# Kernel tuning notes

Measured on AMD Instinct MI355X. Metric: run time of the kernel, lower is better.

## Reference

```python
import jax, jax.numpy as jnp
import numpy as np

D_MODEL = 1024
N_HEADS = 16
HEAD_DIM = D_MODEL // N_HEADS
D_FF = 4096
MAX_STEPS = 16
MAX_LEN = 64  # hardcoded in the module
LN_EPS = 1e-5


def _layer_norm(x, g, b):
    m = jnp.mean(x, axis=-1, keepdims=True)
    v = jnp.mean((x - m) ** 2, axis=-1, keepdims=True)
    return (x - m) * jax.lax.rsqrt(v + LN_EPS) * g + b


def setup_inputs() -> dict:
    key = jax.random.key(0)
    ks = jax.random.split(key, 12)
    B, S = 8, 1024
    std = 0.02
    return {
        "x": jax.random.normal(ks[0], (B, S, D_MODEL), dtype=jnp.float32),
        "step_embed": jax.random.normal(ks[1], (MAX_STEPS, D_MODEL), dtype=jnp.float32) * std,
        "qkv_w": jax.random.normal(ks[2], (D_MODEL, 3 * D_MODEL), dtype=jnp.float32) * std,
        "qkv_b": jnp.zeros((3 * D_MODEL,), dtype=jnp.float32),
        "out_w": jax.random.normal(ks[3], (D_MODEL, D_MODEL), dtype=jnp.float32) * std,
        "out_b": jnp.zeros((D_MODEL,), dtype=jnp.float32),
        "rel_pos_bias": jax.random.normal(ks[4], (2 * MAX_LEN - 1,), dtype=jnp.float32) * std,
        "w1": jax.random.normal(ks[5], (D_MODEL, D_FF), dtype=jnp.float32) * std,
        "b1": jnp.zeros((D_FF,), dtype=jnp.float32),
        "w2": jax.random.normal(ks[6], (D_FF, D_MODEL), dtype=jnp.float32) * std,
        "b2": jnp.zeros((D_MODEL,), dtype=jnp.float32),
        "ln1_g": jnp.ones((D_MODEL,), dtype=jnp.float32),
        "ln1_b": jnp.zeros((D_MODEL,), dtype=jnp.float32),
        "ln2_g": jnp.ones((D_MODEL,), dtype=jnp.float32),
        "ln2_b": jnp.zeros((D_MODEL,), dtype=jnp.float32),
        "think_step": 3,
    }


def reference(x, step_embed, qkv_w, qkv_b, out_w, out_b, rel_pos_bias,
              w1, b1, w2, b2, ln1_g, ln1_b, ln2_g, ln2_b, think_step):
    B, S, D = x.shape
    scale = HEAD_DIM ** -0.5

    # step embedding (clamped), broadcast over batch and sequence
    step = min(int(think_step), MAX_STEPS - 1)
    x = x + step_embed[step][None, None, :]

    # QKV projection -> (3, B, H, S, Dh)
    qkv = (x @ qkv_w + qkv_b).reshape(B, S, 3, N_HEADS, HEAD_DIM)
    qkv = jnp.transpose(qkv, (2, 0, 3, 1, 4))
    q, k, v = qkv[0], qkv[1], qkv[2]

    # attention scores with clamped relative-position bias
    scores = jnp.einsum("bhqd,bhkd->bhqk", q, k) * scale
    pos = jnp.arange(S)
    rel = jnp.clip(pos[:, None] - pos[None, :] + (MAX_LEN - 1), 0, 2 * MAX_LEN - 2)
    scores = scores + rel_pos_bias[rel][None, None, :, :]

    probs = jax.nn.softmax(scores, axis=-1)
    attn = jnp.einsum("bhqk,bhkd->bhqd", probs, v)
    attn = jnp.transpose(attn, (0, 2, 1, 3)).reshape(B, S, D)
    attn = attn @ out_w + out_b

    x = _layer_norm(x + attn, ln1_g, ln1_b)
    ffn = jax.nn.gelu(x @ w1 + b1, approximate=False) @ w2 + b2
    x = _layer_norm(x + ffn, ln2_g, ln2_b)
    return x
```

## Files before the change

### kernel.cpp

```cpp
#include <hip/hip_runtime.h>
#include <cstdint>
#include <cmath>

typedef unsigned short u16;
typedef unsigned int u32;
typedef __bf16 bf16x8 __attribute__((ext_vector_type(8)));
typedef float f32x4 __attribute__((ext_vector_type(4)));
typedef float f32x16 __attribute__((ext_vector_type(16)));

#define DEV __device__ __forceinline__

DEV u16 f2bf(float f) {
    union { float f; unsigned u; } a; a.f = f;
    unsigned u = a.u;
    return (u16)((u + 0x7FFFu + ((u >> 16) & 1u)) >> 16);
}

DEV u32 pack2bf(float a, float b) {
    union { float f; u32 u; } ua, ub; ua.f = a; ub.f = b;
    return __builtin_amdgcn_perm(ub.u + 0x8000u, ua.u + 0x8000u, 0x07060302u);
}

DEV float fast_exp2(float x) {
    float r;
    asm("v_exp_f32 %0, %1" : "=v"(r) : "v"(x));
    return r;
}

DEV void async16(void* lds, const void* g) {
    __builtin_amdgcn_global_load_lds(
        (const __attribute__((address_space(1))) unsigned int*)g,
        (__attribute__((address_space(3))) unsigned int*)lds, 16, 0, 0);
}

#define LOG2E 1.44269504088896f

__global__ void transpose_all(const float* __restrict__ s0, u16* __restrict__ d0,
                              const float* __restrict__ s1, u16* __restrict__ d1,
                              const float* __restrict__ s2, u16* __restrict__ d2,
                              const float* __restrict__ s3, u16* __restrict__ d3) {
    __shared__ float tile[32][33];
    int b = blockIdx.x;
    const float* src; u16* dst; int N, tidx;
    if (b < 3072)      { src = s0; dst = d0; N = 3072; tidx = b; }
    else if (b < 4096) { src = s1; dst = d1; N = 1024; tidx = b - 3072; }
    else if (b < 8192) { src = s2; dst = d2; N = 4096; tidx = b - 4096; }
    else               { src = s3; dst = d3; N = 1024; tidx = b - 8192; }
    int ntx = N >> 5;
    int n0 = (tidx % ntx) * 32, k0 = (tidx / ntx) * 32;
    int K = (b >= 8192) ? 4096 : 1024;
    int tx = threadIdx.x, ty = threadIdx.y;
    #pragma unroll
    for (int i = ty; i < 32; i += 8) tile[i][tx] = src[(size_t)(k0 + i) * N + n0 + tx];
    __syncthreads();
    #pragma unroll
    for (int i = ty; i < 32; i += 8) dst[(size_t)(n0 + i) * K + k0 + tx] = f2bf(tile[tx][i]);
}

__global__ __launch_bounds__(256)
void add_step_k(const float* __restrict__ x, const float* __restrict__ se,
                const int* __restrict__ ts, float* __restrict__ xo, u16* __restrict__ xb) {
    int st = ts[0]; st = st < 0 ? 0 : (st > 15 ? 15 : st);
    size_t i = (size_t)blockIdx.x * 256 + threadIdx.x;
    float4 v = ((const float4*)x)[i];
    int c = (int)(i & 255);
    float4 e = ((const float4*)(se + (size_t)st * 1024))[c];
    v.x += e.x; v.y += e.y; v.z += e.z; v.w += e.w;
    ((float4*)xo)[i] = v;
    ushort4 u; u.x = f2bf(v.x); u.y = f2bf(v.y); u.z = f2bf(v.z); u.w = f2bf(v.w);
    ((ushort4*)xb)[i] = u;
}

template<int EPI>
__global__ __launch_bounds__(256)
void gemm_bt(const u16* __restrict__ A, const u16* __restrict__ Bt,
             const float* __restrict__ bias, int Kdim,
             u16* __restrict__ ob0, u16* __restrict__ ob1, u16* __restrict__ ob2,
             const float* __restrict__ addf, float* __restrict__ outf) {
    __shared__ __align__(16) u16 lA[128 * 64];
    __shared__ __align__(16) u16 lB[128 * 64];
    const int tid = threadIdx.x, wave = tid >> 6, lane = tid & 63;
    const int m5 = lane & 31, h = lane >> 5;
    const int wm = wave >> 1, wn = wave & 1;
    const size_t m0 = (size_t)blockIdx.x * 128, n0 = (size_t)blockIdx.y * 128;
    const size_t kb = (size_t)Kdim * 2;

    f32x16 acc[2][2];
    #pragma unroll
    for (int i = 0; i < 2; i++)
        #pragma unroll
        for (int j = 0; j < 2; j++)
            #pragma unroll
            for (int e = 0; e < 16; e++) acc[i][j][e] = 0.f;

    const char* Ab = (const char*)A + m0 * kb;
    const char* Bb = (const char*)Bt + n0 * kb;

    auto stage = [&](const char* srcbase, u16* ldsb, int k0) {
        #pragma unroll
        for (int j = 0; j < 4; j++) {
            int loff = wave * 4096 + j * 1024 + lane * 16;
            int L = loff >> 4, r = L >> 3, c = L & 7, g = c ^ (r & 7);
            async16((char*)ldsb + loff, srcbase + (size_t)r * kb + (size_t)k0 * 2 + g * 16);
        }
    };

    stage(Ab, lA, 0); stage(Bb, lB, 0);
    const int r7 = m5 & 7;
    for (int k0 = 0; k0 < Kdim; k0 += 64) {
        __syncthreads();
        bf16x8 af[2][4], bfr[2][4];
        #pragma unroll
        for (int ti = 0; ti < 2; ti++) {
            int rowA = wm * 64 + ti * 32 + m5;
            int rowB = wn * 64 + ti * 32 + m5;
            #pragma unroll
            for (int kh = 0; kh < 4; kh++) {
                int cs = (kh * 2 + h) ^ r7;
                af[ti][kh]  = *(const bf16x8*)((const char*)lA + rowA * 128 + cs * 16);
                bfr[ti][kh] = *(const bf16x8*)((const char*)lB + rowB * 128 + cs * 16);
            }
        }
        __syncthreads();
        if (k0 + 64 < Kdim) { stage(Ab, lA, k0 + 64); stage(Bb, lB, k0 + 64); }
        #pragma unroll
        for (int kh = 0; kh < 4; kh++)
            #pragma unroll
            for (int ti = 0; ti < 2; ti++)
                #pragma unroll
                for (int tj = 0; tj < 2; tj++)
                    acc[ti][tj] = __builtin_amdgcn_mfma_f32_32x32x16_bf16(
                        af[ti][kh], bfr[tj][kh], acc[ti][tj], 0, 0, 0);
    }

    #pragma unroll
    for (int ti = 0; ti < 2; ti++) {
        #pragma unroll
        for (int tj = 0; tj < 2; tj++) {
            size_t col = n0 + wn * 64 + tj * 32 + m5;
            float bv = bias[col];
            if constexpr (EPI == 0) {
                size_t t = col >> 10, c = col & 1023, hh = c >> 6, dh = c & 63;
                #pragma unroll
                for (int g = 0; g < 4; g++) {
                    size_t row0 = m0 + wm * 64 + ti * 32 + 4 * h + 8 * g;
                    size_t bq = row0 >> 10, s0 = row0 & 1023;
                    if (t == 0) {
                        #pragma unroll
                        for (int r = 0; r < 4; r++)
                            ob0[((bq * 16 + hh) * 1024 + s0 + r) * 64 + dh] =
                                f2bf((acc[ti][tj][g * 4 + r] + bv) * 0.18033688011112f);
                    } else if (t == 1) {
                        #pragma unroll
                        for (int r = 0; r < 4; r++)
                            ob1[((bq * 16 + hh) * 1024 + s0 + r) * 64 + dh] =
                                f2bf(acc[ti][tj][g * 4 + r] + bv);
                    } else {
                        ushort4 tmp;
                        tmp.x = f2bf(acc[ti][tj][g * 4 + 0] + bv);
                        tmp.y = f2bf(acc[ti][tj][g * 4 + 1] + bv);
                        tmp.z = f2bf(acc[ti][tj][g * 4 + 2] + bv);
                        tmp.w = f2bf(acc[ti][tj][g * 4 + 3] + bv);
                        *(ushort4*)(ob2 + ((bq * 16 + hh) * 64 + dh) * 1024 + s0) = tmp;
                    }
                }
            } else {
                #pragma unroll
                for (int g = 0; g < 4; g++) {
                    #pragma unroll
                    for (int r = 0; r < 4; r++) {
                        size_t row = m0 + wm * 64 + ti * 32 + 4 * h + 8 * g + r;
                        float val = acc[ti][tj][g * 4 + r] + bv;
                        if constexpr (EPI == 1) {
                            size_t o = row * 1024 + col;
                            outf[o] = addf[o] + val;
                        } else if constexpr (EPI == 2) {
                            float ge = 0.5f * val * (1.f + erff(val * 0.70710678118f));
                            ob0[row * 4096 + col] = f2bf(ge);
                        } else {
                            size_t o = row * 1024 + col;
                            outf[o] = addf[o] + val;
                        }
                    }
                }
            }
        }
    }
}

__global__ __launch_bounds__(256)
void attn_k(const u16* __restrict__ Q, const u16* __restrict__ K_, const u16* __restrict__ Vt,
            const float* __restrict__ relb, u16* __restrict__ Out) {
    __shared__ __align__(16) u16 sP[64 * 128];
    __shared__ __align__(16) u16 sK[128 * 64];
    __shared__ __align__(16) u16 sVt[64 * 128];
    __shared__ float sRel[128];

    const int tid = threadIdx.x, wave = tid >> 6, lane = tid & 63;
    const int quad = lane >> 4, l15 = lane & 15;
    const int sw8 = l15 & 7;
    const int bh = blockIdx.x, q0 = blockIdx.y * 64;
    const size_t base = (size_t)bh * 65536;

    if (tid < 127) sRel[tid] = relb[tid] * LOG2E;

    auto stageK = [&](int kv0) {
        const char* kbp = (const char*)(K_ + base + (size_t)kv0 * 64);
        #pragma unroll
        for (int j = 0; j < 4; j++) {
            int loff = wave * 4096 + j * 1024 + lane * 16;
            int L = loff >> 4, r = L >> 3, c = L & 7, g = c ^ (r & 7);
            async16((char*)sK + loff, kbp + (size_t)r * 128 + g * 16);
        }
    };
    auto stageV = [&](int kv0) {
        const char* vbp = (const char*)(Vt + base) + (size_t)kv0 * 2;
        #pragma unroll
        for (int j = 0; j < 4; j++) {
            int loff = wave * 4096 + j * 1024 + lane * 16;
            int L = loff >> 4, r = L >> 4, c = L & 15, g = c ^ (r & 15);
            async16((char*)sVt + loff, vbp + (size_t)r * 2048 + g * 16);
        }
    };

    {
        const char* qb = (const char*)(Q + base + (size_t)q0 * 64);
        #pragma unroll
        for (int j = 0; j < 2; j++) {
            int loff = wave * 2048 + j * 1024 + lane * 16;
            int L = loff >> 4, r = L >> 3, c = L & 7, g = c ^ (r & 7);
            async16((char*)sP + loff, qb + (size_t)r * 128 + g * 16);
        }
    }
    stageK(0); stageV(0);
    __syncthreads();

    const int rowQ = wave * 16 + l15;
    bf16x8 aq0 = *(const bf16x8*)((const char*)sP + rowQ * 128 + ((quad ^ sw8) * 16));
    bf16x8 aq1 = *(const bf16x8*)((const char*)sP + rowQ * 128 + (((4 + quad) ^ sw8) * 16));

    bf16x8 ones;
    {
        union { short s[8]; bf16x8 v; } ou;
        #pragma unroll
        for (int i = 0; i < 8; i++) ou.s[i] = 0x3F80;
        ones = ou.v;
    }

    f32x4 Oacc[4], lsum;
    #pragma unroll
    for (int n = 0; n < 4; n++) Oacc[n] = f32x4{0.f, 0.f, 0.f, 0.f};
    lsum = f32x4{0.f, 0.f, 0.f, 0.f};

    for (int t = 0; t < 8; t++) {
        const int kv0 = t * 128;
        f32x4 sc[8];
        #pragma unroll
        for (int ni = 0; ni < 8; ni++) {
            const char* kr = (const char*)sK + (ni * 16 + l15) * 128;
            bf16x8 k0f = *(const bf16x8*)(kr + ((quad ^ sw8) * 16));
            bf16x8 k1f = *(const bf16x8*)(kr + (((4 + quad) ^ sw8) * 16));
            f32x4 z = f32x4{0.f, 0.f, 0.f, 0.f};
            z = __builtin_amdgcn_mfma_f32_16x16x32_bf16(k0f, aq0, z, 0, 0, 0);
            sc[ni] = __builtin_amdgcn_mfma_f32_16x16x32_bf16(k1f, aq1, z, 0, 0, 0);
        }
        const int qs = q0 + rowQ;
        if (kv0 >= q0 + 126) {
            float cb = sRel[0];
            #pragma unroll
            for (int ni = 0; ni < 8; ni++)
                #pragma unroll
                for (int r = 0; r < 4; r++) sc[ni][r] = fast_exp2(sc[ni][r] + cb);
        } else if (kv0 <= q0 - 190) {
            float cb = sRel[126];
            #pragma unroll
            for (int ni = 0; ni < 8; ni++)
                #pragma unroll
                for (int r = 0; r < 4; r++) sc[ni][r] = fast_exp2(sc[ni][r] + cb);
        } else {
            #pragma unroll
            for (int ni = 0; ni < 8; ni++) {
                #pragma unroll
                for (int r = 0; r < 4; r++) {
                    int ks = kv0 + ni * 16 + quad * 4 + r;
                    int rel = qs - ks + 63;
                    rel = rel < 0 ? 0 : (rel > 126 ? 126 : rel);
                    sc[ni][r] = fast_exp2(sc[ni][r] + sRel[rel]);
                }
            }
        }
        {
            char* prow = (char*)sP + rowQ * 256 + (quad & 1) * 8;
            #pragma unroll
            for (int ni = 0; ni < 8; ni++) {
                uint2 pk;
                pk.x = pack2bf(sc[ni][0], sc[ni][1]);
                pk.y = pack2bf(sc[ni][2], sc[ni][3]);
                int c16 = (ni * 2 + (quad >> 1)) ^ l15;
                *(uint2*)(prow + c16 * 16) = pk;
            }
        }
        __syncthreads();
        if (t < 7) stageK(kv0 + 128);

        #pragma unroll
        for (int kk = 0; kk < 4; kk++) {
            int swc = (kk * 4 + quad) ^ l15;
            bf16x8 pf = *(const bf16x8*)((const char*)sP + rowQ * 256 + swc * 16);
            lsum = __builtin_amdgcn_mfma_f32_16x16x32_bf16(pf, ones, lsum, 0, 0, 0);
            #pragma unroll
            for (int n = 0; n < 4; n++) {
                bf16x8 vf = *(const bf16x8*)((const char*)sVt + (n * 16 + l15) * 256 + swc * 16);
                Oacc[n] = __builtin_amdgcn_mfma_f32_16x16x32_bf16(pf, vf, Oacc[n], 0, 0, 0);
            }
        }
        __syncthreads();
        if (t < 7) stageV(kv0 + 128);
    }

    const int b = bh >> 4, hh = bh & 15;
    #pragma unroll
    for (int r = 0; r < 4; r++) {
        float inv = 1.f / lsum[r];
        int srow = q0 + wave * 16 + quad * 4 + r;
        size_t rowg = ((size_t)b * 1024 + srow) * 1024 + hh * 64;
        #pragma unroll
        for (int n = 0; n < 4; n++) Out[rowg + n * 16 + l15] = f2bf(Oacc[n][r] * inv);
    }
}

template<bool WB>
__global__ __launch_bounds__(256)
void ln_k(const float* __restrict__ in, const float* __restrict__ g, const float* __restrict__ b,
          float* __restrict__ of, u16* __restrict__ ob) {
    __shared__ float ws1[4], ws2[4];
    int row = blockIdx.x, t = threadIdx.x;
    float4 v = ((const float4*)(in + (size_t)row * 1024))[t];
    float s = v.x + v.y + v.z + v.w;
    float s2 = v.x * v.x + v.y * v.y + v.z * v.z + v.w * v.w;
    #pragma unroll
    for (int m = 1; m < 64; m <<= 1) { s += __shfl_xor(s, m); s2 += __shfl_xor(s2, m); }
    if ((t & 63) == 0) { ws1[t >> 6] = s; ws2[t >> 6] = s2; }
    __syncthreads();
    s = ws1[0] + ws1[1] + ws1[2] + ws1[3];
    s2 = ws2[0] + ws2[1] + ws2[2] + ws2[3];
    float mean = s * (1.f / 1024.f);
    float var = s2 * (1.f / 1024.f) - mean * mean;
    float inv = rsqrtf(var + 1e-5f);
    float4 gv = ((const float4*)g)[t], bv = ((const float4*)b)[t];
    float4 o;
    o.x = (v.x - mean) * inv * gv.x + bv.x;
    o.y = (v.y - mean) * inv * gv.y + bv.y;
    o.z = (v.z - mean) * inv * gv.z + bv.z;
    o.w = (v.w - mean) * inv * gv.w + bv.w;
    ((float4*)(of + (size_t)row * 1024))[t] = o;
    if (WB) {
        ushort4 u; u.x = f2bf(o.x); u.y = f2bf(o.y); u.z = f2bf(o.z); u.w = f2bf(o.w);
        ((ushort4*)(ob + (size_t)row * 1024))[t] = u;
    }
}

extern "C" void kernel_launch(void* const* d_in, const int* in_sizes, int n_in,
                              void* d_out, int out_size, void* d_ws, size_t ws_size,
                              hipStream_t stream) {
    (void)in_sizes; (void)n_in; (void)out_size; (void)ws_size;
    const float* x          = (const float*)d_in[0];
    const float* step_embed = (const float*)d_in[1];
    const float* qkv_w      = (const float*)d_in[2];
    const float* qkv_b      = (const float*)d_in[3];
    const float* out_w      = (const float*)d_in[4];
    const float* out_b      = (const float*)d_in[5];
    const float* relb       = (const float*)d_in[6];
    const float* w1         = (const float*)d_in[7];
    const float* b1         = (const float*)d_in[8];
    const float* w2         = (const float*)d_in[9];
    const float* b2         = (const float*)d_in[10];
    const float* ln1g       = (const float*)d_in[11];
    const float* ln1b       = (const float*)d_in[12];
    const float* ln2g       = (const float*)d_in[13];
    const float* ln2b       = (const float*)d_in[14];
    const int*   tstep      = (const int*)d_in[15];
    float* out = (float*)d_out;

    char* p = (char*)d_ws;
    u16* wt_qkv = (u16*)p; p += (size_t)3072 * 1024 * 2;
    u16* wt_out = (u16*)p; p += (size_t)1024 * 1024 * 2;
    u16* wt_w1  = (u16*)p; p += (size_t)4096 * 1024 * 2;
    u16* wt_w2  = (u16*)p; p += (size_t)1024 * 4096 * 2;
    float* xse  = (float*)p; p += (size_t)8192 * 1024 * 4;
    u16* xseb   = (u16*)p; p += (size_t)8192 * 1024 * 2;
    u16* qbuf   = (u16*)p; p += (size_t)8192 * 1024 * 2;
    u16* kbuf   = (u16*)p; p += (size_t)8192 * 1024 * 2;
    u16* attnb  = (u16*)p; p += (size_t)8192 * 1024 * 2;
    float* res1 = (float*)p; p += (size_t)8192 * 1024 * 4;
    float* y1   = xse;
    u16*   y1b  = xseb;
    u16*   hbuf = qbuf;
    float* res2 = res1;
    u16*   vtb  = (u16*)res1;

    transpose_all<<<dim3(12288), dim3(32, 8), 0, stream>>>(qkv_w, wt_qkv, out_w, wt_out,
                                                           w1, wt_w1, w2, wt_w2);
    add_step_k<<<dim3(8192), dim3(256), 0, stream>>>(x, step_embed, tstep, xse, xseb);
    gemm_bt<0><<<dim3(64, 24), dim3(256), 0, stream>>>(xseb, wt_qkv, qkv_b, 1024,
                                                       qbuf, kbuf, vtb, (const float*)nullptr, (float*)nullptr);
    attn_k<<<dim3(128, 16), dim3(256), 0, stream>>>(qbuf, kbuf, vtb, relb, attnb);
    gemm_bt<1><<<dim3(64, 8), dim3(256), 0, stream>>>(attnb, wt_out, out_b, 1024,
                                                      (u16*)nullptr, (u16*)nullptr, (u16*)nullptr, xse, res1);
    ln_k<true><<<dim3(8192), dim3(256), 0, stream>>>(res1, ln1g, ln1b, y1, y1b);
    gemm_bt<2><<<dim3(64, 32), dim3(256), 0, stream>>>(y1b, wt_w1, b1, 1024,
                                                       hbuf, (u16*)nullptr, (u16*)nullptr, (const float*)nullptr, (float*)nullptr);
    gemm_bt<3><<<dim3(64, 8), dim3(256), 0, stream>>>(hbuf, wt_w2, b2, 4096,
                                                      (u16*)nullptr, (u16*)nullptr, (u16*)nullptr, y1, res2);
    ln_k<false><<<dim3(8192), dim3(256), 0, stream>>>(res2, ln2g, ln2b, out, (u16*)nullptr);
}
```

Measured before the change: 530.2 us.

## Restructure attention to 128-query tiles with 32x32 MFMA and merge prep kernels

The attention kernel now processes 128 queries per block instead of 64, halving the grid and the number of times K/V tiles are loaded per head. It switches to 32x32x16 MFMA instructions, splits the work so each wave computes scores for a 32-key slice and later accumulates P·V for a 64-query by 32-dim output slice, and computes row sums directly with a cross-wave LDS reduction. The weight transpose and step-embedding add are fused into one launch to save a kernel launch. Risks are higher register pressure from holding 16 Q fragments and larger LDS use, which could lower occupancy.

```diff
diff --git a/kernel.cpp b/kernel.cpp
--- a/kernel.cpp
+++ b/kernel.cpp
@@ -35,40 +35,41 @@
 
 #define LOG2E 1.44269504088896f
 
-__global__ void transpose_all(const float* __restrict__ s0, u16* __restrict__ d0,
-                              const float* __restrict__ s1, u16* __restrict__ d1,
-                              const float* __restrict__ s2, u16* __restrict__ d2,
-                              const float* __restrict__ s3, u16* __restrict__ d3) {
-    __shared__ float tile[32][33];
-    int b = blockIdx.x;
-    const float* src; u16* dst; int N, tidx;
-    if (b < 3072)      { src = s0; dst = d0; N = 3072; tidx = b; }
-    else if (b < 4096) { src = s1; dst = d1; N = 1024; tidx = b - 3072; }
-    else if (b < 8192) { src = s2; dst = d2; N = 4096; tidx = b - 4096; }
-    else               { src = s3; dst = d3; N = 1024; tidx = b - 8192; }
-    int ntx = N >> 5;
-    int n0 = (tidx % ntx) * 32, k0 = (tidx / ntx) * 32;
-    int K = (b >= 8192) ? 4096 : 1024;
-    int tx = threadIdx.x, ty = threadIdx.y;
-    #pragma unroll
-    for (int i = ty; i < 32; i += 8) tile[i][tx] = src[(size_t)(k0 + i) * N + n0 + tx];
-    __syncthreads();
-    #pragma unroll
-    for (int i = ty; i < 32; i += 8) dst[(size_t)(n0 + i) * K + k0 + tx] = f2bf(tile[tx][i]);
-}
-
 __global__ __launch_bounds__(256)
-void add_step_k(const float* __restrict__ x, const float* __restrict__ se,
-                const int* __restrict__ ts, float* __restrict__ xo, u16* __restrict__ xb) {
-    int st = ts[0]; st = st < 0 ? 0 : (st > 15 ? 15 : st);
-    size_t i = (size_t)blockIdx.x * 256 + threadIdx.x;
-    float4 v = ((const float4*)x)[i];
-    int c = (int)(i & 255);
-    float4 e = ((const float4*)(se + (size_t)st * 1024))[c];
-    v.x += e.x; v.y += e.y; v.z += e.z; v.w += e.w;
-    ((float4*)xo)[i] = v;
-    ushort4 u; u.x = f2bf(v.x); u.y = f2bf(v.y); u.z = f2bf(v.z); u.w = f2bf(v.w);
-    ((ushort4*)xb)[i] = u;
+void prep_k(const float* __restrict__ s0, u16* __restrict__ d0,
+            const float* __restrict__ s1, u16* __restrict__ d1,
+            const float* __restrict__ s2, u16* __restrict__ d2,
+            const float* __restrict__ s3, u16* __restrict__ d3,
+            const float* __restrict__ x, const float* __restrict__ se,
+            const int* __restrict__ ts, float* __restrict__ xo, u16* __restrict__ xb) {
+    int b = blockIdx.x, tid = threadIdx.x;
+    if (b < 12288) {
+        __shared__ float tile[32][33];
+        const float* src; u16* dst; int N, tidx;
+        if (b < 3072)      { src = s0; dst = d0; N = 3072; tidx = b; }
+        else if (b < 4096) { src = s1; dst = d1; N = 1024; tidx = b - 3072; }
+        else if (b < 8192) { src = s2; dst = d2; N = 4096; tidx = b - 4096; }
+        else               { src = s3; dst = d3; N = 1024; tidx = b - 8192; }
+        int ntx = N >> 5;
+        int n0 = (tidx % ntx) * 32, k0 = (tidx / ntx) * 32;
+        int K = (b >= 8192) ? 4096 : 1024;
+        int tx = tid & 31, ty = tid >> 5;
+        #pragma unroll
+        for (int i = ty; i < 32; i += 8) tile[i][tx] = src[(size_t)(k0 + i) * N + n0 + tx];
+        __syncthreads();
+        #pragma unroll
+        for (int i = ty; i < 32; i += 8) dst[(size_t)(n0 + i) * K + k0 + tx] = f2bf(tile[tx][i]);
+    } else {
+        int st = ts[0]; st = st < 0 ? 0 : (st > 15 ? 15 : st);
+        size_t i = (size_t)(b - 12288) * 256 + tid;
+        float4 v = ((const float4*)x)[i];
+        int c = (int)(i & 255);
+        float4 e = ((const float4*)(se + (size_t)st * 1024))[c];
+        v.x += e.x; v.y += e.y; v.z += e.z; v.w += e.w;
+        ((float4*)xo)[i] = v;
+        ushort4 u; u.x = f2bf(v.x); u.y = f2bf(v.y); u.z = f2bf(v.z); u.w = f2bf(v.w);
+        ((ushort4*)xb)[i] = u;
+    }
 }
 
 template<int EPI>
@@ -188,18 +189,19 @@
     }
 }
 
-__global__ __launch_bounds__(256)
+__global__ __launch_bounds__(256, 2)
 void attn_k(const u16* __restrict__ Q, const u16* __restrict__ K_, const u16* __restrict__ Vt,
             const float* __restrict__ relb, u16* __restrict__ Out) {
-    __shared__ __align__(16) u16 sP[64 * 128];
+    __shared__ __align__(16) u16 sP[128 * 128];
     __shared__ __align__(16) u16 sK[128 * 64];
     __shared__ __align__(16) u16 sVt[64 * 128];
+    __shared__ float sL[4][128];
+    __shared__ float sLinv[128];
     __shared__ float sRel[128];
 
     const int tid = threadIdx.x, wave = tid >> 6, lane = tid & 63;
-    const int quad = lane >> 4, l15 = lane & 15;
-    const int sw8 = l15 & 7;
-    const int bh = blockIdx.x, q0 = blockIdx.y * 64;
+    const int m5 = lane & 31, h = lane >> 5;
+    const int bh = blockIdx.x, q0 = blockIdx.y * 128;
     const size_t base = (size_t)bh * 65536;
 
     if (tid < 127) sRel[tid] = relb[tid] * LOG2E;
@@ -226,8 +228,8 @@
     {
         const char* qb = (const char*)(Q + base + (size_t)q0 * 64);
         #pragma unroll
-        for (int j = 0; j < 2; j++) {
-            int loff = wave * 2048 + j * 1024 + lane * 16;
+        for (int j = 0; j < 4; j++) {
+            int loff = wave * 4096 + j * 1024 + lane * 16;
             int L = loff >> 4, r = L >> 3, c = L & 7, g = c ^ (r & 7);
             async16((char*)sP + loff, qb + (size_t)r * 128 + g * 16);
         }
@@ -235,97 +237,134 @@
     stageK(0); stageV(0);
     __syncthreads();
 
-    const int rowQ = wave * 16 + l15;
-    bf16x8 aq0 = *(const bf16x8*)((const char*)sP + rowQ * 128 + ((quad ^ sw8) * 16));
-    bf16x8 aq1 = *(const bf16x8*)((const char*)sP + rowQ * 128 + (((4 + quad) ^ sw8) * 16));
-
-    bf16x8 ones;
-    {
-        union { short s[8]; bf16x8 v; } ou;
-        #pragma unroll
-        for (int i = 0; i < 8; i++) ou.s[i] = 0x3F80;
-        ones = ou.v;
-    }
-
-    f32x4 Oacc[4], lsum;
-    #pragma unroll
-    for (int n = 0; n < 4; n++) Oacc[n] = f32x4{0.f, 0.f, 0.f, 0.f};
-    lsum = f32x4{0.f, 0.f, 0.f, 0.f};
+    bf16x8 qf[4][4];
+    #pragma unroll
+    for (int qt = 0; qt < 4; qt++) {
+        int row = qt * 32 + m5;
+        #pragma unroll
+        for (int s = 0; s < 4; s++) {
+            int cs = (2 * s + h) ^ (m5 & 7);
+            qf[qt][s] = *(const bf16x8*)((const char*)sP + row * 128 + cs * 16);
+        }
+    }
+    __syncthreads();
+
+    const int qh = wave >> 1, dhh = wave & 1;
+    f32x16 Oacc[2];
+    #pragma unroll
+    for (int i = 0; i < 2; i++)
+        #pragma unroll
+        for (int e = 0; e < 16; e++) Oacc[i][e] = 0.f;
+    float lsum[4] = {0.f, 0.f, 0.f, 0.f};
 
     for (int t = 0; t < 8; t++) {
         const int kv0 = t * 128;
-        f32x4 sc[8];
-        #pragma unroll
-        for (int ni = 0; ni < 8; ni++) {
-            const char* kr = (const char*)sK + (ni * 16 + l15) * 128;
-            bf16x8 k0f = *(const bf16x8*)(kr + ((quad ^ sw8) * 16));
-            bf16x8 k1f = *(const bf16x8*)(kr + (((4 + quad) ^ sw8) * 16));
-            f32x4 z = f32x4{0.f, 0.f, 0.f, 0.f};
-            z = __builtin_amdgcn_mfma_f32_16x16x32_bf16(k0f, aq0, z, 0, 0, 0);
-            sc[ni] = __builtin_amdgcn_mfma_f32_16x16x32_bf16(k1f, aq1, z, 0, 0, 0);
-        }
-        const int qs = q0 + rowQ;
-        if (kv0 >= q0 + 126) {
-            float cb = sRel[0];
-            #pragma unroll
-            for (int ni = 0; ni < 8; ni++)
+        const int kvr = wave * 32 + m5;
+        bf16x8 kf[4];
+        #pragma unroll
+        for (int s = 0; s < 4; s++) {
+            int cs = (2 * s + h) ^ (m5 & 7);
+            kf[s] = *(const bf16x8*)((const char*)sK + kvr * 128 + cs * 16);
+        }
+        f32x16 sc[4];
+        #pragma unroll
+        for (int qt = 0; qt < 4; qt++)
+            #pragma unroll
+            for (int e = 0; e < 16; e++) sc[qt][e] = 0.f;
+        #pragma unroll
+        for (int s = 0; s < 4; s++)
+            #pragma unroll
+            for (int qt = 0; qt < 4; qt++)
+                sc[qt] = __builtin_amdgcn_mfma_f32_32x32x16_bf16(kf[s], qf[qt][s], sc[qt], 0, 0, 0);
+
+        const int kvb = kv0 + wave * 32 + 4 * h;
+        const bool far_lo = (kv0 >= q0 + 190);
+        const bool far_hi = (kv0 <= q0 - 190);
+        #pragma unroll
+        for (int qt = 0; qt < 4; qt++) {
+            const int qs = q0 + qt * 32 + m5;
+            if (far_lo || far_hi) {
+                float cb = far_lo ? sRel[0] : sRel[126];
                 #pragma unroll
-                for (int r = 0; r < 4; r++) sc[ni][r] = fast_exp2(sc[ni][r] + cb);
-        } else if (kv0 <= q0 - 190) {
-            float cb = sRel[126];
-            #pragma unroll
-            for (int ni = 0; ni < 8; ni++)
+                for (int e = 0; e < 16; e++) sc[qt][e] = fast_exp2(sc[qt][e] + cb);
+            } else {
+                int relbase = qs - kvb + 63;
                 #pragma unroll
-                for (int r = 0; r < 4; r++) sc[ni][r] = fast_exp2(sc[ni][r] + cb);
-        } else {
-            #pragma unroll
-            for (int ni = 0; ni < 8; ni++) {
-                #pragma unroll
-                for (int r = 0; r < 4; r++) {
-                    int ks = kv0 + ni * 16 + quad * 4 + r;
-                    int rel = qs - ks + 63;
-                    rel = rel < 0 ? 0 : (rel > 126 ? 126 : rel);
-                    sc[ni][r] = fast_exp2(sc[ni][r] + sRel[rel]);
-                }
-            }
-        }
-        {
-            char* prow = (char*)sP + rowQ * 256 + (quad & 1) * 8;
-            #pragma unroll
-            for (int ni = 0; ni < 8; ni++) {
-                uint2 pk;
-                pk.x = pack2bf(sc[ni][0], sc[ni][1]);
-                pk.y = pack2bf(sc[ni][2], sc[ni][3]);
-                int c16 = (ni * 2 + (quad >> 1)) ^ l15;
-                *(uint2*)(prow + c16 * 16) = pk;
+                for (int g = 0; g < 4; g++)
+                    #pragma unroll
+                    for (int r = 0; r < 4; r++) {
+                        int rel = relbase - 8 * g - r;
+                        rel = rel < 0 ? 0 : (rel > 126 ? 126 : rel);
+                        sc[qt][4 * g + r] = fast_exp2(sc[qt][4 * g + r] + sRel[rel]);
+                    }
+            }
+            #pragma unroll
+            for (int e = 0; e < 16; e++) lsum[qt] += sc[qt][e];
+            u32 pk[4][2];
+            #pragma unroll
+            for (int g = 0; g < 4; g++) {
+                pk[g][0] = pack2bf(sc[qt][4 * g + 0], sc[qt][4 * g + 1]);
+                pk[g][1] = pack2bf(sc[qt][4 * g + 2], sc[qt][4 * g + 3]);
+            }
+            const int q = qt * 32 + m5;
+            char* prow = (char*)sP + q * 256;
+            #pragma unroll
+            for (int u = 0; u < 2; u++) {
+                u32 s0 = h ? pk[2 * u][0] : pk[2 * u + 1][0];
+                u32 s1 = h ? pk[2 * u][1] : pk[2 * u + 1][1];
+                u32 r0 = __shfl_xor((int)s0, 32);
+                u32 r1 = __shfl_xor((int)s1, 32);
+                uint4 w;
+                if (h == 0) { w.x = pk[2 * u][0]; w.y = pk[2 * u][1]; w.z = r0; w.w = r1; }
+                else        { w.x = r0; w.y = r1; w.z = pk[2 * u + 1][0]; w.w = pk[2 * u + 1][1]; }
+                int c16 = (4 * wave + 2 * u + h) ^ (q & 15);
+                *(uint4*)(prow + c16 * 16) = w;
             }
         }
         __syncthreads();
         if (t < 7) stageK(kv0 + 128);
 
         #pragma unroll
-        for (int kk = 0; kk < 4; kk++) {
-            int swc = (kk * 4 + quad) ^ l15;
-            bf16x8 pf = *(const bf16x8*)((const char*)sP + rowQ * 256 + swc * 16);
-            lsum = __builtin_amdgcn_mfma_f32_16x16x32_bf16(pf, ones, lsum, 0, 0, 0);
-            #pragma unroll
-            for (int n = 0; n < 4; n++) {
-                bf16x8 vf = *(const bf16x8*)((const char*)sVt + (n * 16 + l15) * 256 + swc * 16);
-                Oacc[n] = __builtin_amdgcn_mfma_f32_16x16x32_bf16(pf, vf, Oacc[n], 0, 0, 0);
+        for (int s = 0; s < 8; s++) {
+            int dh = dhh * 32 + m5;
+            int cv = (2 * s + h) ^ (dh & 15);
+            bf16x8 vf = *(const bf16x8*)((const char*)sVt + dh * 256 + cv * 16);
+            #pragma unroll
+            for (int qt = 0; qt < 2; qt++) {
+                int q = qh * 64 + qt * 32 + m5;
+                int cp = (2 * s + h) ^ (q & 15);
+                bf16x8 pf = *(const bf16x8*)((const char*)sP + q * 256 + cp * 16);
+                Oacc[qt] = __builtin_amdgcn_mfma_f32_32x32x16_bf16(pf, vf, Oacc[qt], 0, 0, 0);
             }
         }
         __syncthreads();
         if (t < 7) stageV(kv0 + 128);
     }
 
+    #pragma unroll
+    for (int qt = 0; qt < 4; qt++) lsum[qt] += __shfl_xor(lsum[qt], 32);
+    if (h == 0) {
+        #pragma unroll
+        for (int qt = 0; qt < 4; qt++) sL[wave][qt * 32 + m5] = lsum[qt];
+    }
+    __syncthreads();
+    if (tid < 128) sLinv[tid] = 1.f / (sL[0][tid] + sL[1][tid] + sL[2][tid] + sL[3][tid]);
+    __syncthreads();
+
     const int b = bh >> 4, hh = bh & 15;
-    #pragma unroll
-    for (int r = 0; r < 4; r++) {
-        float inv = 1.f / lsum[r];
-        int srow = q0 + wave * 16 + quad * 4 + r;
-        size_t rowg = ((size_t)b * 1024 + srow) * 1024 + hh * 64;
-        #pragma unroll
-        for (int n = 0; n < 4; n++) Out[rowg + n * 16 + l15] = f2bf(Oacc[n][r] * inv);
+    const int dh = dhh * 32 + m5;
+    #pragma unroll
+    for (int qt = 0; qt < 2; qt++) {
+        #pragma unroll
+        for (int g = 0; g < 4; g++) {
+            #pragma unroll
+            for (int r = 0; r < 4; r++) {
+                int rl = qh * 64 + qt * 32 + 4 * h + 8 * g + r;
+                float val = Oacc[qt][4 * g + r] * sLinv[rl];
+                size_t s = (size_t)(q0 + rl);
+                Out[((size_t)b * 1024 + s) * 1024 + hh * 64 + dh] = f2bf(val);
+            }
+        }
     }
 }
 
@@ -399,12 +438,12 @@
     float* res2 = res1;
     u16*   vtb  = (u16*)res1;
 
-    transpose_all<<<dim3(12288), dim3(32, 8), 0, stream>>>(qkv_w, wt_qkv, out_w, wt_out,
-                                                           w1, wt_w1, w2, wt_w2);
-    add_step_k<<<dim3(8192), dim3(256), 0, stream>>>(x, step_embed, tstep, xse, xseb);
+    prep_k<<<dim3(12288 + 8192), dim3(256), 0, stream>>>(qkv_w, wt_qkv, out_w, wt_out,
+                                                         w1, wt_w1, w2, wt_w2,
+                                                         x, step_embed, tstep, xse, xseb);
     gemm_bt<0><<<dim3(64, 24), dim3(256), 0, stream>>>(xseb, wt_qkv, qkv_b, 1024,
                                                        qbuf, kbuf, vtb, (const float*)nullptr, (float*)nullptr);
-    attn_k<<<dim3(128, 16), dim3(256), 0, stream>>>(qbuf, kbuf, vtb, relb, attnb);
+    attn_k<<<dim3(128, 8), dim3(256), 0, stream>>>(qbuf, kbuf, vtb, relb, attnb);
     gemm_bt<1><<<dim3(64, 8), dim3(256), 0, stream>>>(attnb, wt_out, out_b, 1024,
                                                       (u16*)nullptr, (u16*)nullptr, (u16*)nullptr, xse, res1);
     ln_k<true><<<dim3(8192), dim3(256), 0, stream>>>(res1, ln1g, ln1b, y1, y1b);
```

Result: no change. 522.9 us (-1.4%).
